# Kernel tuning notes

Measured on AMD Instinct MI355X. Metric: run time of the kernel, lower is better.

## Reference

```python
import jax, jax.numpy as jnp
import numpy as np

B, T, NT = 256, 1024, 96  # batch, max seq len, num_tags (incl. start/end)


def setup_inputs() -> dict:
    key = jax.random.key(0)
    k1, k2, k3 = jax.random.split(key, 3)
    h = jax.random.normal(k1, (B, T, NT), dtype=jnp.float32)
    # lengths in [1, T]; force at least one full-length sequence so max_len == T
    lengths = jax.random.randint(k2, (B,), 1, T + 1).at[0].set(T)
    trans = jax.random.normal(k3, (NT, NT), dtype=jnp.float32)  # trans[to, from]
    return {"h": h, "lengths": lengths, "trans": trans}


def reference(h, lengths, trans):
    # CRF forward algorithm (log partition function), masked for variable lengths.
    Bb, Tt, nt = h.shape
    start_tag, end_tag = nt - 2, nt - 1  # start_tag=-2, end_tag=-1
    mask = jnp.arange(Tt)[None, :] < lengths[:, None]  # [B, T]

    score0 = jnp.full((Bb, nt), -10000.0, dtype=h.dtype).at[:, start_tag].set(0.0)

    def step(score, xs):
        h_t, m_t = xs  # h_t: [B, NT], m_t: [B]
        # score[b, j] (prev tag j) + trans[i, j] + emit h_t[b, i] -> [B, NT(i), NT(j)]
        s = score[:, None, :] + trans[None, :, :] + h_t[:, :, None]
        s = jax.nn.logsumexp(s, axis=2)  # [B, NT]
        score = jnp.where(m_t[:, None], s, score)
        return score, None

    score, _ = jax.lax.scan(step, score0, (jnp.swapaxes(h, 0, 1), mask.T))
    # transition into end tag, then final logsumexp over tags -> [B]
    return jax.nn.logsumexp(score + trans[end_tag][None, :], axis=1)
```

## Files before the change

kernel.cpp:

```cpp
#include <hip/hip_runtime.h>

#define Bb 256
#define Tt 1024
#define NT 96
#define PF 8

__global__ __launch_bounds__(256, 1) void crf_fwd_kernel(
    const float* __restrict__ h,
    const int*   __restrict__ lengths,
    const float* __restrict__ trans,
    float* __restrict__ out)
{
    const int b    = blockIdx.x;
    const int tid  = threadIdx.x;
    const int i    = tid >> 1;
    const int q    = tid & 1;
    const int L    = lengths[b];
    const bool active = (i < NT);
    const int wave = tid >> 6;

    __shared__ float p_lds[2][128];
    __shared__ float fin[4];

    float E[48];
    if (active) {
        const float* tr = trans + i * NT + q * 48;
        #pragma unroll
        for (int k = 0; k < 48; ++k) E[k] = __expf(tr[k]);
    } else {
        #pragma unroll
        for (int k = 0; k < 48; ++k) E[k] = 0.0f;
    }

    if (tid < 128) p_lds[0][tid] = (tid == NT - 2) ? 1.0f : 0.0f;

    const float* hb = h + (size_t)b * Tt * NT;

    float hp[PF];
    #pragma unroll
    for (int k = 0; k < PF; ++k)
        hp[k] = active ? hb[(size_t)k * NT + i] : 0.0f;

    const float c  = 4.0f;
    const float Kc = __expf(-c);
    float M = 0.0f;
    float p_keep = 0.0f;

    __syncthreads();

    int cur = 0;
    for (int tb = 0; tb < Tt; tb += PF) {
        #pragma unroll
        for (int k = 0; k < PF; ++k) {
            const int t = tb + k;

            const float p0 = p_lds[cur][0];

            const float4* pv = reinterpret_cast<const float4*>(p_lds[cur] + q * 48);
            float a0 = 0.f, a1 = 0.f, a2 = 0.f, a3 = 0.f;
            #pragma unroll
            for (int m = 0; m < 12; ++m) {
                const float4 p4 = pv[m];
                a0 = fmaf(E[4*m+0], p4.x, a0);
                a1 = fmaf(E[4*m+1], p4.y, a1);
                a2 = fmaf(E[4*m+2], p4.z, a2);
                a3 = fmaf(E[4*m+3], p4.w, a3);
            }
            float v = (a0 + a1) + (a2 + a3);
            v += __shfl_xor(v, 1, 64);

            const float eh = __expf(hp[k]);
            int tn = t + PF; if (tn > Tt - 1) tn = Tt - 1;
            hp[k] = active ? hb[(size_t)tn * NT + i] : 0.0f;

            const float u  = (t == 0) ? 1.0f : Kc * __builtin_amdgcn_rcpf(p0);
            const float w  = v * eh;
            const bool msk = (t < L);
            const float pn = msk ? (w * u) : p_keep;
            M -= msk ? __logf(u) : 0.0f;
            p_keep = pn;

            const int nxt = cur ^ 1;
            if (active && q == 0) p_lds[nxt][i] = pn;

            __syncthreads();
            cur = nxt;
        }
    }

    float term = (active && q == 0) ? p_keep * __expf(trans[(NT - 1) * NT + i]) : 0.0f;
    #pragma unroll
    for (int s = 1; s < 64; s <<= 1) term += __shfl_xor(term, s, 64);
    if ((tid & 63) == 0) fin[wave] = term;
    __syncthreads();
    if (tid == 0) out[b] = M + __logf(fin[0] + fin[1] + fin[2] + fin[3]);
}

extern "C" void kernel_launch(void* const* d_in, const int* in_sizes, int n_in,
                              void* d_out, int out_size, void* d_ws, size_t ws_size,
                              hipStream_t stream) {
    const float* h       = (const float*)d_in[0];
    const int*   lengths = (const int*)d_in[1];
    const float* trans   = (const float*)d_in[2];
    float*       out     = (float*)d_out;
    (void)in_sizes; (void)n_in; (void)out_size; (void)d_ws; (void)ws_size;

    crf_fwd_kernel<<<Bb, 256, 0, stream>>>(h, lengths, trans, out);
}
```

Before: 405.5 us.

## Double-buffer emission prefetch and replace syncthreads with LDS-only barrier

Splits the emission prefetch into two register banks so a batch of global loads is issued after each 8-step group and has a full group to land. It also replaces __syncthreads with an explicit lgkmcnt(0) wait plus s_barrier. That way the per-step barrier no longer waits on outstanding global loads (vmcnt), only on LDS traffic. Inactive threads load a valid address instead of branching. This doubles the prefetch register footprint and relies on the hand-written barrier being correct.

```diff
diff --git a/kernel.cpp b/kernel.cpp
--- a/kernel.cpp
+++ b/kernel.cpp
@@ -34,12 +34,14 @@
 
     if (tid < 128) p_lds[0][tid] = (tid == NT - 2) ? 1.0f : 0.0f;
 
-    const float* hb = h + (size_t)b * Tt * NT;
+    const float* hb  = h + (size_t)b * Tt * NT;
+    const float* hld = active ? (hb + i) : hb;
 
-    float hp[PF];
+    float hpA[PF], hpB[PF];
     #pragma unroll
-    for (int k = 0; k < PF; ++k)
-        hp[k] = active ? hb[(size_t)k * NT + i] : 0.0f;
+    for (int k = 0; k < PF; ++k) hpA[k] = hld[(size_t)k * NT];
+    #pragma unroll
+    for (int k = 0; k < PF; ++k) hpB[k] = hld[(size_t)(PF + k) * NT];
 
     const float c  = 4.0f;
     const float Kc = __expf(-c);
@@ -49,44 +51,56 @@
     __syncthreads();
 
     int cur = 0;
-    for (int tb = 0; tb < Tt; tb += PF) {
+
+#define STEP(HREG, T_)                                                        \
+    {                                                                         \
+        const float p0 = p_lds[cur][0];                                       \
+        const float4* pv = reinterpret_cast<const float4*>(p_lds[cur] + q*48);\
+        float a0 = 0.f, a1 = 0.f, a2 = 0.f, a3 = 0.f;                         \
+        _Pragma("unroll")                                                     \
+        for (int m_ = 0; m_ < 12; ++m_) {                                     \
+            const float4 p4 = pv[m_];                                         \
+            a0 = fmaf(E[4*m_+0], p4.x, a0);                                   \
+            a1 = fmaf(E[4*m_+1], p4.y, a1);                                   \
+            a2 = fmaf(E[4*m_+2], p4.z, a2);                                   \
+            a3 = fmaf(E[4*m_+3], p4.w, a3);                                   \
+        }                                                                     \
+        float v = (a0 + a1) + (a2 + a3);                                      \
+        v += __shfl_xor(v, 1, 64);                                            \
+        const float eh = __expf(HREG);                                        \
+        const float u  = ((T_) == 0) ? 1.0f : Kc * __builtin_amdgcn_rcpf(p0); \
+        const float w  = v * eh;                                              \
+        const bool msk = ((T_) < L);                                          \
+        const float pn = msk ? (w * u) : p_keep;                              \
+        M -= msk ? __logf(u) : 0.0f;                                          \
+        p_keep = pn;                                                          \
+        if (active && q == 0) p_lds[cur ^ 1][i] = pn;                         \
+        asm volatile("s_waitcnt lgkmcnt(0)" ::: "memory");                    \
+        __builtin_amdgcn_s_barrier();                                         \
+        asm volatile("" ::: "memory");                                        \
+        cur ^= 1;                                                             \
+    }
+
+    for (int tb = 0; tb < Tt; tb += 2 * PF) {
         #pragma unroll
-        for (int k = 0; k < PF; ++k) {
-            const int t = tb + k;
+        for (int k = 0; k < PF; ++k) STEP(hpA[k], tb + k);
 
-            const float p0 = p_lds[cur][0];
+        #pragma unroll
+        for (int m = 0; m < PF; ++m) {
+            int tn = tb + 2 * PF + m; if (tn > Tt - 1) tn = Tt - 1;
+            hpA[m] = hld[(size_t)tn * NT];
+        }
 
-            const float4* pv = reinterpret_cast<const float4*>(p_lds[cur] + q * 48);
-            float a0 = 0.f, a1 = 0.f, a2 = 0.f, a3 = 0.f;
-            #pragma unroll
-            for (int m = 0; m < 12; ++m) {
-                const float4 p4 = pv[m];
-                a0 = fmaf(E[4*m+0], p4.x, a0);
-                a1 = fmaf(E[4*m+1], p4.y, a1);
-                a2 = fmaf(E[4*m+2], p4.z, a2);
-                a3 = fmaf(E[4*m+3], p4.w, a3);
-            }
-            float v = (a0 + a1) + (a2 + a3);
-            v += __shfl_xor(v, 1, 64);
+        #pragma unroll
+        for (int k = 0; k < PF; ++k) STEP(hpB[k], tb + PF + k);
 
-            const float eh = __expf(hp[k]);
-            int tn = t + PF; if (tn > Tt - 1) tn = Tt - 1;
-            hp[k] = active ? hb[(size_t)tn * NT + i] : 0.0f;
-
-            const float u  = (t == 0) ? 1.0f : Kc * __builtin_amdgcn_rcpf(p0);
-            const float w  = v * eh;
-            const bool msk = (t < L);
-            const float pn = msk ? (w * u) : p_keep;
-            M -= msk ? __logf(u) : 0.0f;
-            p_keep = pn;
-
-            const int nxt = cur ^ 1;
-            if (active && q == 0) p_lds[nxt][i] = pn;
-
-            __syncthreads();
-            cur = nxt;
+        #pragma unroll
+        for (int m = 0; m < PF; ++m) {
+            int tn = tb + 3 * PF + m; if (tn > Tt - 1) tn = Tt - 1;
+            hpB[m] = hld[(size_t)tn * NT];
         }
     }
+#undef STEP
 
     float term = (active && q == 0) ? p_keep * __expf(trans[(NT - 1) * NT + i]) : 0.0f;
     #pragma unroll
```

After: 382.3 us. -5.7%, faster.

## Run each sequence in a single wavefront and drop per-step block barriers

Applied to the files above, without the earlier changes.

Each batch element now runs in one 64-lane wavefront instead of 256 threads. Each lane computes one full tag row (tags 0-63) plus half of one of the remaining 32 rows, with the exponentiated transitions pinned in registers. Because the block is a single wave, the per-timestep __syncthreads and the cross-wave final reduction are removed, which takes barrier latency off the serial recurrence. In exchange each lane does about three times the FMA work per step and holds 144 transition values in registers. LDS visibility between steps now depends only on in-wave ordering.

```diff
diff --git a/kernel.cpp b/kernel.cpp
--- a/kernel.cpp
+++ b/kernel.cpp
@@ -3,97 +3,132 @@
 #define Bb 256
 #define Tt 1024
 #define NT 96
-#define PF 8
+#define PF 4
 
-__global__ __launch_bounds__(256, 1) void crf_fwd_kernel(
+__global__ __attribute__((amdgpu_flat_work_group_size(64, 64),
+                          amdgpu_waves_per_eu(1, 1)))
+void crf_fwd_kernel(
     const float* __restrict__ h,
     const int*   __restrict__ lengths,
     const float* __restrict__ trans,
     float* __restrict__ out)
 {
-    const int b    = blockIdx.x;
-    const int tid  = threadIdx.x;
-    const int i    = tid >> 1;
-    const int q    = tid & 1;
-    const int L    = lengths[b];
-    const bool active = (i < NT);
-    const int wave = tid >> 6;
+    const int b   = blockIdx.x;
+    const int l   = threadIdx.x;
+    const int par = l & 1;
+    const int r2  = 64 + (l >> 1);
+    const int L   = lengths[b];
 
     __shared__ float p_lds[2][128];
-    __shared__ float fin[4];
 
-    float E[48];
-    if (active) {
-        const float* tr = trans + i * NT + q * 48;
+    float EA[96], EB[48];
+    {
+        const float4* ra = reinterpret_cast<const float4*>(trans + l * NT);
         #pragma unroll
-        for (int k = 0; k < 48; ++k) E[k] = __expf(tr[k]);
-    } else {
+        for (int m = 0; m < 24; ++m) {
+            const float4 t4 = ra[m];
+            EA[4*m+0] = __expf(t4.x); EA[4*m+1] = __expf(t4.y);
+            EA[4*m+2] = __expf(t4.z); EA[4*m+3] = __expf(t4.w);
+        }
+        const float4* rb = reinterpret_cast<const float4*>(trans + r2 * NT + par * 48);
         #pragma unroll
-        for (int k = 0; k < 48; ++k) E[k] = 0.0f;
+        for (int m = 0; m < 12; ++m) {
+            const float4 t4 = rb[m];
+            EB[4*m+0] = __expf(t4.x); EB[4*m+1] = __expf(t4.y);
+            EB[4*m+2] = __expf(t4.z); EB[4*m+3] = __expf(t4.w);
+        }
+    }
+#define PIN12(A,B,C,D,E_,F,G,H,I,J,K,Lq) \
+    asm volatile("" : "+v"(A), "+v"(B), "+v"(C), "+v"(D), "+v"(E_), "+v"(F), \
+                      "+v"(G), "+v"(H), "+v"(I), "+v"(J), "+v"(K), "+v"(Lq));
+    PIN12(EA[0],EA[1],EA[2],EA[3],EA[4],EA[5],EA[6],EA[7],EA[8],EA[9],EA[10],EA[11])
+    PIN12(EA[12],EA[13],EA[14],EA[15],EA[16],EA[17],EA[18],EA[19],EA[20],EA[21],EA[22],EA[23])
+    PIN12(EA[24],EA[25],EA[26],EA[27],EA[28],EA[29],EA[30],EA[31],EA[32],EA[33],EA[34],EA[35])
+    PIN12(EA[36],EA[37],EA[38],EA[39],EA[40],EA[41],EA[42],EA[43],EA[44],EA[45],EA[46],EA[47])
+    PIN12(EA[48],EA[49],EA[50],EA[51],EA[52],EA[53],EA[54],EA[55],EA[56],EA[57],EA[58],EA[59])
+    PIN12(EA[60],EA[61],EA[62],EA[63],EA[64],EA[65],EA[66],EA[67],EA[68],EA[69],EA[70],EA[71])
+    PIN12(EA[72],EA[73],EA[74],EA[75],EA[76],EA[77],EA[78],EA[79],EA[80],EA[81],EA[82],EA[83])
+    PIN12(EA[84],EA[85],EA[86],EA[87],EA[88],EA[89],EA[90],EA[91],EA[92],EA[93],EA[94],EA[95])
+    PIN12(EB[0],EB[1],EB[2],EB[3],EB[4],EB[5],EB[6],EB[7],EB[8],EB[9],EB[10],EB[11])
+    PIN12(EB[12],EB[13],EB[14],EB[15],EB[16],EB[17],EB[18],EB[19],EB[20],EB[21],EB[22],EB[23])
+    PIN12(EB[24],EB[25],EB[26],EB[27],EB[28],EB[29],EB[30],EB[31],EB[32],EB[33],EB[34],EB[35])
+    PIN12(EB[36],EB[37],EB[38],EB[39],EB[40],EB[41],EB[42],EB[43],EB[44],EB[45],EB[46],EB[47])
+#undef PIN12
+
+    p_lds[0][l] = 0.0f;
+    if (l < 32) p_lds[0][64 + l] = (l == 30) ? 1.0f : 0.0f;
+
+    const float* hA = h + (size_t)b * Tt * NT + l;
+    const float* hB = h + (size_t)b * Tt * NT + r2;
+    float hpA[PF], hpB[PF];
+    #pragma unroll
+    for (int k = 0; k < PF; ++k) {
+        hpA[k] = hA[(size_t)k * NT];
+        hpB[k] = hB[(size_t)k * NT];
     }
 
-    if (tid < 128) p_lds[0][tid] = (tid == NT - 2) ? 1.0f : 0.0f;
+    const float Kc = __expf(-4.0f);
+    float M = 0.0f, pkA = 0.0f, pkB = 0.0f;
+    int cur = 0;
 
-    const float* hb = h + (size_t)b * Tt * NT;
-
-    float hp[PF];
-    #pragma unroll
-    for (int k = 0; k < PF; ++k)
-        hp[k] = active ? hb[(size_t)k * NT + i] : 0.0f;
-
-    const float c  = 4.0f;
-    const float Kc = __expf(-c);
-    float M = 0.0f;
-    float p_keep = 0.0f;
-
-    __syncthreads();
-
-    int cur = 0;
     for (int tb = 0; tb < Tt; tb += PF) {
         #pragma unroll
         for (int k = 0; k < PF; ++k) {
             const int t = tb + k;
+            const float* pc = p_lds[cur];
+            const float4* pa4 = reinterpret_cast<const float4*>(pc);
+            const float4* pb4 = reinterpret_cast<const float4*>(pc + par * 48);
 
-            const float p0 = p_lds[cur][0];
-
-            const float4* pv = reinterpret_cast<const float4*>(p_lds[cur] + q * 48);
-            float a0 = 0.f, a1 = 0.f, a2 = 0.f, a3 = 0.f;
+            const float4 q0 = pa4[0];
+            const float p0 = q0.x;
+            float a0 = EA[0]*q0.x, a1 = EA[1]*q0.y, a2 = EA[2]*q0.z, a3 = EA[3]*q0.w;
+            #pragma unroll
+            for (int m = 1; m < 24; ++m) {
+                const float4 p4 = pa4[m];
+                a0 = fmaf(EA[4*m+0], p4.x, a0);
+                a1 = fmaf(EA[4*m+1], p4.y, a1);
+                a2 = fmaf(EA[4*m+2], p4.z, a2);
+                a3 = fmaf(EA[4*m+3], p4.w, a3);
+            }
+            float b0 = 0.f, b1 = 0.f, b2 = 0.f, b3 = 0.f;
             #pragma unroll
             for (int m = 0; m < 12; ++m) {
-                const float4 p4 = pv[m];
-                a0 = fmaf(E[4*m+0], p4.x, a0);
-                a1 = fmaf(E[4*m+1], p4.y, a1);
-                a2 = fmaf(E[4*m+2], p4.z, a2);
-                a3 = fmaf(E[4*m+3], p4.w, a3);
+                const float4 p4 = pb4[m];
+                b0 = fmaf(EB[4*m+0], p4.x, b0);
+                b1 = fmaf(EB[4*m+1], p4.y, b1);
+                b2 = fmaf(EB[4*m+2], p4.z, b2);
+                b3 = fmaf(EB[4*m+3], p4.w, b3);
             }
-            float v = (a0 + a1) + (a2 + a3);
-            v += __shfl_xor(v, 1, 64);
+            const float vA  = (a0 + a1) + (a2 + a3);
+            const float vBh = (b0 + b1) + (b2 + b3);
+            const float vB  = vBh + __shfl_xor(vBh, 1, 64);
 
-            const float eh = __expf(hp[k]);
+            const float u   = (t == 0) ? 1.0f : Kc * __builtin_amdgcn_rcpf(p0);
+            const float ehA = __expf(hpA[k]);
+            const float ehB = __expf(hpB[k]);
             int tn = t + PF; if (tn > Tt - 1) tn = Tt - 1;
-            hp[k] = active ? hb[(size_t)tn * NT + i] : 0.0f;
+            hpA[k] = hA[(size_t)tn * NT];
+            hpB[k] = hB[(size_t)tn * NT];
 
-            const float u  = (t == 0) ? 1.0f : Kc * __builtin_amdgcn_rcpf(p0);
-            const float w  = v * eh;
             const bool msk = (t < L);
-            const float pn = msk ? (w * u) : p_keep;
-            M -= msk ? __logf(u) : 0.0f;
-            p_keep = pn;
+            const float wA = vA * ehA * u;
+            const float wB = vB * ehB * u;
+            pkA = msk ? wA : pkA;
+            pkB = msk ? wB : pkB;
+            M  -= msk ? __logf(u) : 0.0f;
 
             const int nxt = cur ^ 1;
-            if (active && q == 0) p_lds[nxt][i] = pn;
-
-            __syncthreads();
+            p_lds[nxt][l] = pkA;
+            if (par == 0) p_lds[nxt][r2] = pkB;
             cur = nxt;
         }
     }
 
-    float term = (active && q == 0) ? p_keep * __expf(trans[(NT - 1) * NT + i]) : 0.0f;
+    float term = pkA * __expf(trans[(NT - 1) * NT + l]);
+    if (par == 0) term += pkB * __expf(trans[(NT - 1) * NT + r2]);
     #pragma unroll
     for (int s = 1; s < 64; s <<= 1) term += __shfl_xor(term, s, 64);
-    if ((tid & 63) == 0) fin[wave] = term;
-    __syncthreads();
-    if (tid == 0) out[b] = M + __logf(fin[0] + fin[1] + fin[2] + fin[3]);
+    if (l == 0) out[b] = M + __logf(term);
 }
 
 extern "C" void kernel_launch(void* const* d_in, const int* in_sizes, int n_in,
@@ -105,5 +140,5 @@
     float*       out     = (float*)d_out;
     (void)in_sizes; (void)n_in; (void)out_size; (void)d_ws; (void)ws_size;
 
-    crf_fwd_kernel<<<Bb, 256, 0, stream>>>(h, lengths, trans, out);
+    crf_fwd_kernel<<<Bb, 64, 0, stream>>>(h, lengths, trans, out);
 }
```

After: 612.5 us. 51.1% more time.

## Remap CRF recurrence to 128 threads with three rows per 4-lane group

Applied to the files above, without the earlier changes.

Work is redistributed so each group of 4 lanes computes three output tags, each lane holding 24 columns of three transition rows. This shrinks the block from 256 to 128 threads (two waves), which cuts barrier cost and removes idle lanes. The __syncthreads call is replaced by an explicit lgkmcnt wait plus s_barrier, and asm constraints pin the E arrays in registers. Costs: a longer serial FMA chain per lane, an extra shuffle round, and a prefetch depth reduced from 8 to 4 steps.

```diff
diff --git a/kernel.cpp b/kernel.cpp
--- a/kernel.cpp
+++ b/kernel.cpp
@@ -3,9 +3,11 @@
 #define Bb 256
 #define Tt 1024
 #define NT 96
-#define PF 8
+#define PF 4
 
-__global__ __launch_bounds__(256, 1) void crf_fwd_kernel(
+__global__ __attribute__((amdgpu_flat_work_group_size(128, 128),
+                          amdgpu_waves_per_eu(1, 1)))
+void crf_fwd_kernel(
     const float* __restrict__ h,
     const int*   __restrict__ lengths,
     const float* __restrict__ trans,
@@ -13,38 +15,67 @@
 {
     const int b    = blockIdx.x;
     const int tid  = threadIdx.x;
-    const int i    = tid >> 1;
-    const int q    = tid & 1;
+    const int g    = tid >> 2;
+    const int cg   = tid & 3;
+    const int r0   = g, r1 = 32 + g, r2 = 64 + g;
     const int L    = lengths[b];
-    const bool active = (i < NT);
     const int wave = tid >> 6;
 
-    __shared__ float p_lds[2][128];
-    __shared__ float fin[4];
+    __shared__ float p_lds[2][96];
+    __shared__ float fin[2];
 
-    float E[48];
-    if (active) {
-        const float* tr = trans + i * NT + q * 48;
+    float E0[24], E1[24], E2[24];
+    {
+        const float4* a = reinterpret_cast<const float4*>(trans + r0 * NT + cg * 24);
+        const float4* c = reinterpret_cast<const float4*>(trans + r1 * NT + cg * 24);
+        const float4* d = reinterpret_cast<const float4*>(trans + r2 * NT + cg * 24);
         #pragma unroll
-        for (int k = 0; k < 48; ++k) E[k] = __expf(tr[k]);
-    } else {
+        for (int m = 0; m < 6; ++m) {
+            float4 t4 = a[m];
+            E0[4*m+0]=__expf(t4.x); E0[4*m+1]=__expf(t4.y);
+            E0[4*m+2]=__expf(t4.z); E0[4*m+3]=__expf(t4.w);
+        }
         #pragma unroll
-        for (int k = 0; k < 48; ++k) E[k] = 0.0f;
+        for (int m = 0; m < 6; ++m) {
+            float4 t4 = c[m];
+            E1[4*m+0]=__expf(t4.x); E1[4*m+1]=__expf(t4.y);
+            E1[4*m+2]=__expf(t4.z); E1[4*m+3]=__expf(t4.w);
+        }
+        #pragma unroll
+        for (int m = 0; m < 6; ++m) {
+            float4 t4 = d[m];
+            E2[4*m+0]=__expf(t4.x); E2[4*m+1]=__expf(t4.y);
+            E2[4*m+2]=__expf(t4.z); E2[4*m+3]=__expf(t4.w);
+        }
+    }
+#define PIN12(A) \
+    asm volatile("" : "+v"(A[0]), "+v"(A[1]), "+v"(A[2]),  "+v"(A[3]), \
+                      "+v"(A[4]), "+v"(A[5]), "+v"(A[6]),  "+v"(A[7]), \
+                      "+v"(A[8]), "+v"(A[9]), "+v"(A[10]), "+v"(A[11]));
+#define PIN12H(A) \
+    asm volatile("" : "+v"(A[12]), "+v"(A[13]), "+v"(A[14]), "+v"(A[15]), \
+                      "+v"(A[16]), "+v"(A[17]), "+v"(A[18]), "+v"(A[19]), \
+                      "+v"(A[20]), "+v"(A[21]), "+v"(A[22]), "+v"(A[23]));
+    PIN12(E0) PIN12H(E0) PIN12(E1) PIN12H(E1) PIN12(E2) PIN12H(E2)
+#undef PIN12
+#undef PIN12H
+
+    if (tid < 96) p_lds[0][tid] = (tid == 94) ? 1.0f : 0.0f;
+
+    const float* hbase = h + (size_t)b * Tt * NT;
+    const float* hA = hbase + r0;
+    const float* hB = hbase + r1;
+    const float* hC = hbase + r2;
+    float hp0[PF], hp1[PF], hp2[PF];
+    #pragma unroll
+    for (int k = 0; k < PF; ++k) {
+        hp0[k] = hA[(size_t)k * NT];
+        hp1[k] = hB[(size_t)k * NT];
+        hp2[k] = hC[(size_t)k * NT];
     }
 
-    if (tid < 128) p_lds[0][tid] = (tid == NT - 2) ? 1.0f : 0.0f;
-
-    const float* hb = h + (size_t)b * Tt * NT;
-
-    float hp[PF];
-    #pragma unroll
-    for (int k = 0; k < PF; ++k)
-        hp[k] = active ? hb[(size_t)k * NT + i] : 0.0f;
-
-    const float c  = 4.0f;
-    const float Kc = __expf(-c);
-    float M = 0.0f;
-    float p_keep = 0.0f;
+    const float Kc = __expf(-4.0f);
+    float M = 0.0f, pk0 = 0.0f, pk1 = 0.0f, pk2 = 0.0f;
 
     __syncthreads();
 
@@ -53,47 +84,70 @@
         #pragma unroll
         for (int k = 0; k < PF; ++k) {
             const int t = tb + k;
+            const float p0 = p_lds[cur][0];
+            const float4* pv = reinterpret_cast<const float4*>(p_lds[cur] + cg * 24);
 
-            const float p0 = p_lds[cur][0];
+            float a0=0.f, a1=0.f, b0=0.f, b1=0.f, c0=0.f, c1=0.f;
+            #pragma unroll
+            for (int m = 0; m < 6; ++m) {
+                const float4 p4 = pv[m];
+                a0 = fmaf(E0[4*m+0], p4.x, a0);
+                a1 = fmaf(E0[4*m+1], p4.y, a1);
+                a0 = fmaf(E0[4*m+2], p4.z, a0);
+                a1 = fmaf(E0[4*m+3], p4.w, a1);
+                b0 = fmaf(E1[4*m+0], p4.x, b0);
+                b1 = fmaf(E1[4*m+1], p4.y, b1);
+                b0 = fmaf(E1[4*m+2], p4.z, b0);
+                b1 = fmaf(E1[4*m+3], p4.w, b1);
+                c0 = fmaf(E2[4*m+0], p4.x, c0);
+                c1 = fmaf(E2[4*m+1], p4.y, c1);
+                c0 = fmaf(E2[4*m+2], p4.z, c0);
+                c1 = fmaf(E2[4*m+3], p4.w, c1);
+            }
+            float v0 = a0 + a1, v1 = b0 + b1, v2 = c0 + c1;
+            v0 += __shfl_xor(v0, 1, 64); v0 += __shfl_xor(v0, 2, 64);
+            v1 += __shfl_xor(v1, 1, 64); v1 += __shfl_xor(v1, 2, 64);
+            v2 += __shfl_xor(v2, 1, 64); v2 += __shfl_xor(v2, 2, 64);
 
-            const float4* pv = reinterpret_cast<const float4*>(p_lds[cur] + q * 48);
-            float a0 = 0.f, a1 = 0.f, a2 = 0.f, a3 = 0.f;
-            #pragma unroll
-            for (int m = 0; m < 12; ++m) {
-                const float4 p4 = pv[m];
-                a0 = fmaf(E[4*m+0], p4.x, a0);
-                a1 = fmaf(E[4*m+1], p4.y, a1);
-                a2 = fmaf(E[4*m+2], p4.z, a2);
-                a3 = fmaf(E[4*m+3], p4.w, a3);
-            }
-            float v = (a0 + a1) + (a2 + a3);
-            v += __shfl_xor(v, 1, 64);
+            const float u   = (t == 0) ? 1.0f : Kc * __builtin_amdgcn_rcpf(p0);
+            const float eh0 = __expf(hp0[k]);
+            const float eh1 = __expf(hp1[k]);
+            const float eh2 = __expf(hp2[k]);
+            int tn = t + PF; if (tn > Tt - 1) tn = Tt - 1;
+            hp0[k] = hA[(size_t)tn * NT];
+            hp1[k] = hB[(size_t)tn * NT];
+            hp2[k] = hC[(size_t)tn * NT];
 
-            const float eh = __expf(hp[k]);
-            int tn = t + PF; if (tn > Tt - 1) tn = Tt - 1;
-            hp[k] = active ? hb[(size_t)tn * NT + i] : 0.0f;
-
-            const float u  = (t == 0) ? 1.0f : Kc * __builtin_amdgcn_rcpf(p0);
-            const float w  = v * eh;
             const bool msk = (t < L);
-            const float pn = msk ? (w * u) : p_keep;
-            M -= msk ? __logf(u) : 0.0f;
-            p_keep = pn;
+            pk0 = msk ? v0 * eh0 * u : pk0;
+            pk1 = msk ? v1 * eh1 * u : pk1;
+            pk2 = msk ? v2 * eh2 * u : pk2;
+            M  -= msk ? __logf(u) : 0.0f;
 
             const int nxt = cur ^ 1;
-            if (active && q == 0) p_lds[nxt][i] = pn;
-
-            __syncthreads();
+            if (cg == 0) {
+                p_lds[nxt][r0] = pk0;
+                p_lds[nxt][r1] = pk1;
+                p_lds[nxt][r2] = pk2;
+            }
+            asm volatile("s_waitcnt lgkmcnt(0)" ::: "memory");
+            __builtin_amdgcn_s_barrier();
+            asm volatile("" ::: "memory");
             cur = nxt;
         }
     }
 
-    float term = (active && q == 0) ? p_keep * __expf(trans[(NT - 1) * NT + i]) : 0.0f;
+    float term = 0.0f;
+    if (cg == 0) {
+        term = pk0 * __expf(trans[95 * NT + r0])
+             + pk1 * __expf(trans[95 * NT + r1])
+             + pk2 * __expf(trans[95 * NT + r2]);
+    }
     #pragma unroll
     for (int s = 1; s < 64; s <<= 1) term += __shfl_xor(term, s, 64);
     if ((tid & 63) == 0) fin[wave] = term;
     __syncthreads();
-    if (tid == 0) out[b] = M + __logf(fin[0] + fin[1] + fin[2] + fin[3]);
+    if (tid == 0) out[b] = M + __logf(fin[0] + fin[1]);
 }
 
 extern "C" void kernel_launch(void* const* d_in, const int* in_sizes, int n_in,
@@ -105,5 +159,5 @@
     float*       out     = (float*)d_out;
     (void)in_sizes; (void)n_in; (void)out_size; (void)d_ws; (void)ws_size;
 
-    crf_fwd_kernel<<<Bb, 256, 0, stream>>>(h, lengths, trans, out);
+    crf_fwd_kernel<<<Bb, 128, 0, stream>>>(h, lengths, trans, out);
 }
```

Measured after the change: 390.2 us. 3.8% less time.
